# Performance work log

Measured on AMD Instinct MI355X. Metric: run time of the kernel, lower is better.

The kernel has to match this reference:

```python
import jax, jax.numpy as jnp
import numpy as np

NUM_PERSISTENT = 16
ALIBI_ALPHA = 1.0
START_I = 0
DILATION = 1
LN_EPS = 1e-5


def setup_inputs() -> dict:
    key = jax.random.key(0)
    ks = jax.random.split(key, 16)
    B, S, C, H = 8, 1024, 512, 8
    D = C // H
    P = NUM_PERSISTENT
    Kk = 3
    x = jax.random.normal(ks[0], (B, S, C), dtype=jnp.float32)
    mask = jnp.ones((B, 1, S, S), dtype=jnp.int32)
    sc = 0.02
    Wq = jax.random.normal(ks[1], (D, D), jnp.float32) * sc
    Wk = jax.random.normal(ks[2], (D, D), jnp.float32) * sc
    Wv = jax.random.normal(ks[3], (D, D), jnp.float32) * sc
    pk = jax.random.normal(ks[4], (P, H, D), jnp.float32) * sc
    pv = jax.random.normal(ks[5], (P, H, D), jnp.float32) * sc
    th_pre = jax.random.normal(ks[6], (H, H), jnp.float32) * (1.0 / np.sqrt(H))
    th_post = jax.random.normal(ks[7], (H, H), jnp.float32) * (1.0 / np.sqrt(H))
    fc_w = jax.random.normal(ks[8], (C, C), jnp.float32) * sc
    fc_b = jnp.zeros((C,), jnp.float32)
    conv1_w = jax.random.normal(ks[9], (C, C, Kk), jnp.float32) * 0.01
    conv1_b = jnp.zeros((C,), jnp.float32)
    conv2_w = jax.random.normal(ks[10], (C, C, Kk), jnp.float32) * 0.01
    conv2_b = jnp.zeros((C,), jnp.float32)
    ln_g = jnp.ones((C,), jnp.float32)
    ln_b = jnp.zeros((C,), jnp.float32)
    return dict(x=x, mask=mask, Wq=Wq, Wk=Wk, Wv=Wv, pk=pk, pv=pv,
                th_pre=th_pre, th_post=th_post, fc_w=fc_w, fc_b=fc_b,
                conv1_w=conv1_w, conv1_b=conv1_b, conv2_w=conv2_w,
                conv2_b=conv2_b, ln_g=ln_g, ln_b=ln_b)


def _causal_conv(x_nct, w_oik, b_o, dilation):
    # padding (k-1)*d on both sides + chomp right == pad left only
    k = w_oik.shape[-1]
    p = (k - 1) * dilation
    y = jax.lax.conv_general_dilated(
        x_nct, w_oik, window_strides=(1,), padding=[(p, 0)],
        rhs_dilation=(dilation,), dimension_numbers=("NCH", "OIH", "NCH"))
    return y + b_o[None, :, None]


def reference(x, mask, Wq, Wk, Wv, pk, pv, th_pre, th_post, fc_w, fc_b,
              conv1_w, conv1_b, conv2_w, conv2_b, ln_g, ln_b):
    N, S, C = x.shape
    H = th_pre.shape[0]
    D = C // H
    P = pk.shape[0]

    # ---- MultiHeadAttention (eval: dropout = identity) ----
    xh = x.reshape(N, S, H, D)
    q = jnp.einsum("nshd,ed->nshe", xh, Wq)
    k = jnp.einsum("nshd,ed->nshe", xh, Wk)
    v = jnp.einsum("nshd,ed->nshe", xh, Wv)
    # persistent memory tokens appended along key/value length
    k = jnp.concatenate([k, jnp.broadcast_to(pk[None], (N, P, H, D))], axis=1)
    v = jnp.concatenate([v, jnp.broadcast_to(pv[None], (N, P, H, D))], axis=1)

    energy = jnp.einsum("nqhd,nkhd->nhqk", q, k)  # (N,H,S,S+P)

    # ALiBi bias (symmetric |q-k|), zero over persistent keys
    slopes = 2.0 ** (-(ALIBI_ALPHA * (jnp.arange(1, H + 1, dtype=jnp.float32) + START_I)))
    t = jnp.arange(S, dtype=jnp.float32)
    dist = jnp.abs(t[:, None] - t[None, :])  # (S,S)
    bias = -dist[None, None] * slopes[None, :, None, None]  # (1,H,S,S)
    bias = jnp.pad(bias, ((0, 0), (0, 0), (0, 0), (0, P)))
    energy = energy + bias

    # pre-softmax talking heads (1x1 conv over head axis)
    energy = jnp.einsum("hg,ngqk->nhqk", th_pre, energy)

    ext_mask = jnp.pad(mask, ((0, 0), (0, 0), (0, 0), (0, P)), constant_values=1)
    energy = jnp.where(ext_mask == 0, jnp.float32(-1e4), energy)

    attn = jax.nn.softmax(energy / jnp.sqrt(jnp.float32(C)), axis=-1)
    attn = jnp.einsum("hg,ngqk->nhqk", th_post, attn)

    att_out = jnp.einsum("nhql,nlhd->nqhd", attn, v).reshape(N, S, C)
    att_out = att_out @ fc_w.T + fc_b

    x = x + att_out  # residual (dropout1 identity in eval)

    # ---- TemporalBlock (causal dilated convs, no SE since heads>0) ----
    xc = jnp.transpose(x, (0, 2, 1))  # (N,C,S)
    h = jax.nn.relu(_causal_conv(xc, conv1_w, conv1_b, DILATION))
    h = jax.nn.relu(_causal_conv(h, conv2_w, conv2_b, DILATION))
    out = jax.nn.relu(h + xc)  # downsample is None (in==out)

    # mask out invalid frames
    conv_mask = mask[:, 0, :, 0][:, None, :]  # (N,1,S)
    out = jnp.where(conv_mask == 0, 0.0, out)

    y = jnp.transpose(out, (0, 2, 1))  # (N,S,C)
    mu = jnp.mean(y, axis=-1, keepdims=True)
    var = jnp.mean(jnp.square(y - mu), axis=-1, keepdims=True)
    y = (y - mu) * jax.lax.rsqrt(var + LN_EPS) * ln_g + ln_b
    return y
```

## Files before the change

kernel.cpp:

```cpp
#include <hip/hip_runtime.h>
#include <hip/hip_bf16.h>

#define BN 8
#define SS 1024
#define CC 512
#define HH 8
#define DD 64
#define PP 16
#define KT 1040

typedef __hip_bfloat16 bf16;
typedef unsigned char uchar;
typedef unsigned short ushort;
typedef __attribute__((ext_vector_type(8))) short short8;
typedef __attribute__((ext_vector_type(4))) float f32x4;
typedef __attribute__((ext_vector_type(2))) float f32x2;

__device__ __forceinline__ short f2s(float v){ bf16 b = __float2bfloat16(v); return *(short*)&b; }
__device__ __forceinline__ float s2f(short s){ bf16 b; *(short*)&b = s; return __bfloat162float(b); }
__device__ __forceinline__ uchar f2q(float v){
    return (uchar)__builtin_amdgcn_cvt_pk_fp8_f32(v, v, 0, false);
}

#define MFMA16(a,b,c)  __builtin_amdgcn_mfma_f32_16x16x32_bf16(a,b,c,0,0,0)
#define MFMAF8(a,b,c)  __builtin_amdgcn_mfma_f32_16x16x32_fp8_fp8(a,b,c,0,0,0)

__global__ __launch_bounds__(256) void prep_kernel(
    const float* __restrict__ fc_w, const float* __restrict__ c1w,
    const float* __restrict__ c2w, const float* __restrict__ Wq,
    const float* __restrict__ Wk, const float* __restrict__ Wv,
    const float* __restrict__ th_post,
    short* __restrict__ Bfc, uchar* __restrict__ Bc1,
    uchar* __restrict__ Bc2, short* __restrict__ Bqkv)
{
    int i = blockIdx.x*256 + threadIdx.x;
    const int NFC = 512*512, NCV = 512*1536, NQ = 3*64*64;
    if (i < NFC) {
        int c = i >> 9, r = i & 511;
        int g = r >> 6, d = r & 63;
        float s = 0.f;
        #pragma unroll
        for (int h = 0; h < 8; ++h)
            s += fc_w[(size_t)c*512 + h*64 + d] * th_post[h*8 + g];
        Bfc[i] = f2s(s);
        return;
    }
    i -= NFC;
    if (i < NCV) {
        int o = i/1536, r = i%1536, dk = r>>9, ci = r&511;
        Bc1[i] = f2q(c1w[(o*512+ci)*3+dk] * 16.f); return;
    }
    i -= NCV;
    if (i < NCV) {
        int o = i/1536, r = i%1536, dk = r>>9, ci = r&511;
        Bc2[i] = f2q(c2w[(o*512+ci)*3+dk] * 16.f); return;
    }
    i -= NCV;
    if (i < NQ) {
        int w = i >> 12, rest = i & 4095;
        const float* W = (w==0)?Wq:(w==1)?Wk:Wv;
        Bqkv[i] = f2s(W[((rest>>6)&63)*64 + (rest&63)]);
    }
}

__global__ __launch_bounds__(256) void qkv_mfma(
    const float* __restrict__ x, const short* __restrict__ Bqkv,
    uchar* __restrict__ qf, uchar* __restrict__ kf, short* __restrict__ vf)
{
    __shared__ short Xs[64*72];
    __shared__ short Ws[192*72];
    const int tid = threadIdx.x;
    const int m0 = blockIdx.x * 64;
    const int h = blockIdx.y;
    const int wave = tid >> 6, lane = tid & 63;
    const int lr = lane & 15, lq = lane >> 4;

    for (int i = tid; i < 1024; i += 256) {
        int r = i >> 4, cg = (i & 15)*4;
        float4 v = *(const float4*)(x + (size_t)(m0+r)*CC + h*64 + cg);
        Xs[r*72+cg+0] = f2s(v.x); Xs[r*72+cg+1] = f2s(v.y);
        Xs[r*72+cg+2] = f2s(v.z); Xs[r*72+cg+3] = f2s(v.w);
    }
    for (int i = tid; i < 3072; i += 256) {
        int r = i >> 4, cg = (i & 15)*4;
        *(short4*)(Ws + r*72 + cg) = *(const short4*)(Bqkv + (size_t)r*64 + cg);
    }
    __syncthreads();

    f32x4 acc[12];
    #pragma unroll
    for (int nt = 0; nt < 12; ++nt) acc[nt] = {0.f,0.f,0.f,0.f};
    #pragma unroll
    for (int ks = 0; ks < 2; ++ks) {
        int ko = ks*32 + lq*8;
        short8 a = *(const short8*)(Xs + (wave*16 + lr)*72 + ko);
        #pragma unroll
        for (int nt = 0; nt < 12; ++nt) {
            short8 b = *(const short8*)(Ws + (nt*16 + lr)*72 + ko);
            acc[nt] = MFMA16(a, b, acc[nt]);
        }
    }
    #pragma unroll
    for (int nt = 0; nt < 12; ++nt) {
        int ep = nt*16 + lr;
        int w = ep >> 6, e = ep & 63;
        #pragma unroll
        for (int reg = 0; reg < 4; ++reg) {
            int m = m0 + wave*16 + lq*4 + reg;
            int n = m >> 10, s = m & 1023;
            float v = acc[nt][reg];
            if (w == 0)      qf[((size_t)(n*HH+h)*SS + s)*DD + e] = f2q(v);
            else if (w == 1) kf[((size_t)(n*HH+h)*KT + s)*DD + e] = f2q(v);
            else             vf[((size_t)(n*HH+h)*KT + s)*DD + e] = f2s(v);
        }
    }
}

__global__ __launch_bounds__(256) void persist_kernel(
    const float* __restrict__ pk, const float* __restrict__ pv,
    uchar* __restrict__ kf, short* __restrict__ vf)
{
    int idx = blockIdx.x*256 + threadIdx.x;
    if (idx >= BN*HH*PP*DD) return;
    int d = idx & 63, p = (idx >> 6) & 15, h = (idx >> 10) & 7, n = idx >> 13;
    size_t dst = (((size_t)(n*HH+h))*KT + SS + p)*DD + d;
    size_t src = ((size_t)p*HH + h)*DD + d;
    kf[dst] = f2q(pk[src]);
    vf[dst] = f2s(pv[src]);
}

__global__ __launch_bounds__(256) void vtrans_kernel(
    const short* __restrict__ vf, uchar* __restrict__ vt)
{
    __shared__ short Ts[64*65];
    const int tid = threadIdx.x;
    const int k0 = blockIdx.x * 64;
    const int nh = blockIdx.y;
    for (int i = tid; i < 1024; i += 256) {
        int kk = i >> 4, dg = (i & 15)*4;
        int k = k0 + kk;
        short4 v = {0,0,0,0};
        if (k < KT) v = *(const short4*)(vf + ((size_t)nh*KT + k)*DD + dg);
        Ts[(dg+0)*65 + kk] = v.x;
        Ts[(dg+1)*65 + kk] = v.y;
        Ts[(dg+2)*65 + kk] = v.z;
        Ts[(dg+3)*65 + kk] = v.w;
    }
    __syncthreads();
    for (int i = tid; i < 1024; i += 256) {
        int d = i >> 4, kg = (i & 15)*4;
        int k = k0 + kg;
        if (k < KT) {
            float f0 = s2f(Ts[d*65 + kg+0]), f1 = s2f(Ts[d*65 + kg+1]);
            float f2 = s2f(Ts[d*65 + kg+2]), f3 = s2f(Ts[d*65 + kg+3]);
            int p0 = __builtin_amdgcn_cvt_pk_fp8_f32(f0, f1, 0, false);
            int p1 = __builtin_amdgcn_cvt_pk_fp8_f32(f2, f3, 0, false);
            unsigned int w = (unsigned int)(p0 & 0xffff) | ((unsigned int)p1 << 16);
            *(unsigned int*)(vt + ((size_t)nh*DD + d)*KT + k) = w;
        }
    }
}

__global__ __launch_bounds__(256) void energy_mfma8(
    const uchar* __restrict__ qf, const uchar* __restrict__ kf,
    uchar* __restrict__ E)
{
    __shared__ uchar Qs[64*72];
    __shared__ uchar Ks[64*72];
    const int tid = threadIdx.x;
    const int kt = blockIdx.x;
    const int mt = blockIdx.y;
    const int nh = blockIdx.z;
    const int wave = tid >> 6, lane = tid & 63;
    const int lr = lane & 15, lq = lane >> 4;

    #pragma unroll
    for (int j = 0; j < 2; ++j) {
        int i = tid + j*256;
        int r = i >> 3, c8 = (i & 7)*8;
        *(uint2*)(Qs + r*72 + c8) =
            *(const uint2*)(qf + ((size_t)nh*SS + mt*64 + r)*DD + c8);
        int kcol = kt*64 + r;
        uint2 kv = {0u, 0u};
        if (kcol < KT)
            kv = *(const uint2*)(kf + ((size_t)nh*KT + kcol)*DD + c8);
        *(uint2*)(Ks + r*72 + c8) = kv;
    }
    __syncthreads();

    f32x4 acc[4];
    #pragma unroll
    for (int nt = 0; nt < 4; ++nt) acc[nt] = {0.f,0.f,0.f,0.f};
    #pragma unroll
    for (int ks = 0; ks < 2; ++ks) {
        int ko = ks*32 + lq*8;
        long a = *(const long*)(Qs + (wave*16 + lr)*72 + ko);
        #pragma unroll
        for (int nt = 0; nt < 4; ++nt) {
            long b = *(const long*)(Ks + (nt*16 + lr)*72 + ko);
            acc[nt] = MFMAF8(a, b, acc[nt]);
        }
    }
    const int n = nh >> 3, h = nh & 7;
    #pragma unroll
    for (int nt = 0; nt < 4; ++nt) {
        int kcol = kt*64 + nt*16 + lr;
        if (kcol >= KT) continue;
        #pragma unroll
        for (int reg = 0; reg < 4; ++reg) {
            int q = mt*64 + wave*16 + lq*4 + reg;
            E[(((size_t)(n*SS + q))*HH + h)*KT + kcol] = f2q(acc[nt][reg]);
        }
    }
}

__global__ __launch_bounds__(256) void softmax_kernel(
    uchar* __restrict__ E, const int* __restrict__ mask,
    const float* __restrict__ th_pre)
{
    __shared__ float thp[64];
    __shared__ float wred[4][8];
    const int tid = threadIdx.x;
    const int wave = tid >> 6, lane = tid & 63;
    const int blk = blockIdx.x;
    const int n = blk >> 10, q = blk & 1023;
    const float invs = 0.044194173824159216f;
    const float l2e  = 1.4426950408889634f;
    if (tid < 64) thp[tid] = th_pre[tid]*(invs*l2e);
    __syncthreads();
    uchar* Eb = E + (size_t)blk*HH*KT;

    const float sl[8] = {0.5f,0.25f,0.125f,0.0625f,
                         0.03125f,0.015625f,0.0078125f,0.00390625f};
    const int* mrow = mask + (size_t)n*SS*SS + (size_t)q*SS;

    f32x2 tp[2][8];
    float tl[8];
    float sm[8];
    #pragma unroll
    for (int g = 0; g < 8; ++g) { sm[g] = 0.f; tl[g] = 0.f; }

    #pragma unroll
    for (int jj = 0; jj < 2; ++jj) {
        const int k0 = (tid + jj*256)*2;
        const int2 mk = *(const int2*)(mrow + k0);
        const f32x2 dist = { fabsf((float)(q - k0)), fabsf((float)(q - k0 - 1)) };
        f32x2 a[8];
        #pragma unroll
        for (int g = 0; g < 8; ++g) {
            ushort u = *(const ushort*)(Eb + g*KT + k0);
            f32x2 raw = __builtin_amdgcn_cvt_pk_f32_fp8((int)u, false);
            a[g].x = raw.x - dist.x*sl[g];
            a[g].y = raw.y - dist.y*sl[g];
        }
        #pragma unroll
        for (int h = 0; h < 8; ++h) {
            f32x2 t = {0.f, 0.f};
            #pragma unroll
            for (int g = 0; g < 8; ++g) {
                float c = thp[h*8 + g];
                t.x = fmaf(c, a[g].x, t.x);
                t.y = fmaf(c, a[g].y, t.y);
            }
            f32x2 e;
            e.x = (mk.x == 0) ? 0.f : exp2f(t.x);
            e.y = (mk.y == 0) ? 0.f : exp2f(t.y);
            tp[jj][h] = e;
            sm[h] += e.x + e.y;
        }
    }
    if (tid < 16) {
        const int k = 1024 + tid;
        float a[8];
        #pragma unroll
        for (int g = 0; g < 8; ++g) {
            f32x2 r = __builtin_amdgcn_cvt_pk_f32_fp8((int)Eb[g*KT + k], false);
            a[g] = r.x;
        }
        #pragma unroll
        for (int h = 0; h < 8; ++h) {
            float t = 0.f;
            #pragma unroll
            for (int g = 0; g < 8; ++g) t = fmaf(thp[h*8 + g], a[g], t);
            float e = exp2f(t);
            tl[h] = e;
            sm[h] += e;
        }
    }
    #pragma unroll
    for (int g = 0; g < 8; ++g) {
        #pragma unroll
        for (int off = 32; off > 0; off >>= 1)
            sm[g] += __shfl_xor(sm[g], off);
    }
    if (lane == 0) {
        #pragma unroll
        for (int g = 0; g < 8; ++g) wred[wave][g] = sm[g];
    }
    __syncthreads();
    float lred[8];
    #pragma unroll
    for (int g = 0; g < 8; ++g)
        lred[g] = 1.0f / (wred[0][g] + wred[1][g] + wred[2][g] + wred[3][g]);

    #pragma unroll
    for (int jj = 0; jj < 2; ++jj) {
        const int k0 = (tid + jj*256)*2;
        #pragma unroll
        for (int g = 0; g < 8; ++g) {
            int p = __builtin_amdgcn_cvt_pk_fp8_f32(
                tp[jj][g].x * lred[g], tp[jj][g].y * lred[g], 0, false);
            *(ushort*)(Eb + g*KT + k0) = (ushort)p;
        }
    }
    if (tid < 16) {
        const int k = 1024 + tid;
        #pragma unroll
        for (int g = 0; g < 8; ++g)
            Eb[g*KT + k] = f2q(tl[g] * lred[g]);
    }
}

__device__ __forceinline__ void pv_loadP(const uchar* __restrict__ E,
    int n, int h, int ql0, int kt, int tid, uint2* rp)
{
    int r = tid >> 3, cg = (tid & 7)*8;
    int k = kt*64 + cg;
    uint2 v = {0u, 0u};
    if (k < KT)
        v = *(const uint2*)(E + (((size_t)(n*SS + ql0 + r))*HH + h)*KT + k);
    rp[0] = v;
}
__device__ __forceinline__ void pv_loadV(const uchar* __restrict__ vt,
    int nh, int kt, int tid, uint2* rv)
{
    #pragma unroll
    for (int j = 0; j < 2; ++j) {
        int i = tid + j*256;
        int r = i >> 3, cg = (i & 7)*8;
        int k = kt*64 + cg;
        uint2 v = {0u, 0u};
        if (k < KT)
            v = *(const uint2*)(vt + ((size_t)nh*DD + r)*KT + k);
        rv[j] = v;
    }
}

__global__ __launch_bounds__(256) void pv_mfma(
    const uchar* __restrict__ E, const uchar* __restrict__ vt,
    short* __restrict__ AO)
{
    __shared__ uchar Ps[32*72];
    __shared__ uchar Vs[64*72];
    const int tid = threadIdx.x;
    const int ql0 = blockIdx.x * 32;
    const int nh = blockIdx.y;
    const int n = nh >> 3, h = nh & 7;
    const int wave = tid >> 6, lane = tid & 63;
    const int lr = lane & 15, lq = lane >> 4;
    const int mh = wave & 1, nb = (wave >> 1)*32;

    uint2 rp[1], rv[2];
    pv_loadP(E, n, h, ql0, 0, tid, rp);
    pv_loadV(vt, nh, 0, tid, rv);

    f32x4 acc[2];
    acc[0] = {0.f,0.f,0.f,0.f}; acc[1] = {0.f,0.f,0.f,0.f};

    for (int kt = 0; kt < 17; ++kt) {
        if (kt) __syncthreads();
        {
            int r = tid >> 3, cg = (tid & 7)*8;
            *(uint2*)(Ps + r*72 + cg) = rp[0];
        }
        #pragma unroll
        for (int j = 0; j < 2; ++j) {
            int i = tid + j*256;
            *(uint2*)(Vs + (i >> 3)*72 + (i & 7)*8) = rv[j];
        }
        __syncthreads();
        if (kt + 1 < 17) {
            pv_loadP(E, n, h, ql0, kt+1, tid, rp);
            pv_loadV(vt, nh, kt+1, tid, rv);
        }
        #pragma unroll
        for (int ks = 0; ks < 2; ++ks) {
            int ko = ks*32 + lq*8;
            long a = *(const long*)(Ps + (mh*16 + lr)*72 + ko);
            #pragma unroll
            for (int nt = 0; nt < 2; ++nt) {
                long b = *(const long*)(Vs + (nb + nt*16 + lr)*72 + ko);
                acc[nt] = MFMAF8(a, b, acc[nt]);
            }
        }
    }
    #pragma unroll
    for (int nt = 0; nt < 2; ++nt) {
        int d = nb + nt*16 + lr;
        #pragma unroll
        for (int reg = 0; reg < 4; ++reg) {
            int qg = ql0 + mh*16 + lq*4 + reg;
            AO[((size_t)(n*SS) + qg)*CC + h*64 + d] = f2s(acc[nt][reg]);
        }
    }
}

__device__ __forceinline__ void g_load4(const short* __restrict__ src,
    size_t rowstride, int row0, int col0, int tid, short4* r)
{
    #pragma unroll
    for (int j = 0; j < 4; ++j) {
        int i = tid + j*256;
        int rr = i >> 4, cg = (i & 15)*4;
        r[j] = *(const short4*)(src + (size_t)(row0 + rr)*rowstride + col0 + cg);
    }
}
__device__ __forceinline__ void lds_store4(short* __restrict__ dst,
    int tid, const short4* r)
{
    #pragma unroll
    for (int j = 0; j < 4; ++j) {
        int i = tid + j*256;
        *(short4*)(dst + (i >> 4)*72 + (i & 15)*4) = r[j];
    }
}

__global__ __launch_bounds__(256) void fc_mfma(
    const short* __restrict__ A, const short* __restrict__ Bt,
    const float* __restrict__ bias, const float* __restrict__ x,
    short* __restrict__ out, uchar* __restrict__ out8)
{
    __shared__ short As[64*72];
    __shared__ short Bs[64*72];
    const int tid = threadIdx.x;
    const int lin = blockIdx.x + 8*blockIdx.y;
    const int xcd = lin & 7, slot = lin >> 3;
    const int m0 = (xcd*16 + (slot & 15))*64;
    const int n0 = (slot >> 4)*64;
    const int wave = tid >> 6, lane = tid & 63;
    const int lr = lane & 15, lq = lane >> 4;

    short4 ra[4], rb[4];
    g_load4(A, CC, m0, 0, tid, ra);
    g_load4(Bt, CC, n0, 0, tid, rb);

    f32x4 acc[4];
    #pragma unroll
    for (int nt = 0; nt < 4; ++nt) acc[nt] = {0.f,0.f,0.f,0.f};

    for (int kt = 0; kt < CC; kt += 64) {
        if (kt) __syncthreads();
        lds_store4(As, tid, ra);
        lds_store4(Bs, tid, rb);
        __syncthreads();
        if (kt + 64 < CC) {
            g_load4(A, CC, m0, kt+64, tid, ra);
            g_load4(Bt, CC, n0, kt+64, tid, rb);
        }
        #pragma unroll
        for (int ks = 0; ks < 2; ++ks) {
            int ko = ks*32 + lq*8;
            short8 a = *(const short8*)(As + (wave*16 + lr)*72 + ko);
            #pragma unroll
            for (int nt = 0; nt < 4; ++nt) {
                short8 b = *(const short8*)(Bs + (nt*16 + lr)*72 + ko);
                acc[nt] = MFMA16(a, b, acc[nt]);
            }
        }
    }
    #pragma unroll
    for (int nt = 0; nt < 4; ++nt) {
        int nn = n0 + nt*16 + lr;
        #pragma unroll
        for (int reg = 0; reg < 4; ++reg) {
            int m = m0 + wave*16 + lq*4 + reg;
            float v = acc[nt][reg] + bias[nn] + x[(size_t)m*CC + nn];
            out[(size_t)m*CC + nn]  = f2s(v);
            out8[(size_t)m*CC + nn] = f2q(v);
        }
    }
}

__device__ __forceinline__ void conv_loadA8(const uchar* __restrict__ A,
    int m0, int kt, int tid, uint2* ra)
{
    const int shift = (kt >> 9) - 2;
    const int ci0 = kt & 511;
    #pragma unroll
    for (int j = 0; j < 2; ++j) {
        int i = tid + j*256;
        int rr = i >> 3, c8 = (i & 7)*8;
        int m = m0 + rr;
        int s = m & (SS-1);
        uint2 v = {0u, 0u};
        if (s + shift >= 0)
            v = *(const uint2*)(A + (size_t)(m + shift)*CC + ci0 + c8);
        ra[j] = v;
    }
}
__device__ __forceinline__ void g_load8(const uchar* __restrict__ src,
    size_t rowstride, int row0, int col0, int tid, uint2* r)
{
    #pragma unroll
    for (int j = 0; j < 2; ++j) {
        int i = tid + j*256;
        int rr = i >> 3, c8 = (i & 7)*8;
        r[j] = *(const uint2*)(src + (size_t)(row0 + rr)*rowstride + col0 + c8);
    }
}
__device__ __forceinline__ void lds_store8(uchar* __restrict__ dst,
    int tid, const uint2* r)
{
    #pragma unroll
    for (int j = 0; j < 2; ++j) {
        int i = tid + j*256;
        *(uint2*)(dst + (i >> 3)*72 + (i & 7)*8) = r[j];
    }
}

__global__ __launch_bounds__(256) void conv_mfma8(
    const uchar* __restrict__ A, const uchar* __restrict__ Bt,
    const float* __restrict__ bias, uchar* __restrict__ out8,
    short* __restrict__ out16, int f8out)
{
    __shared__ uchar As[64*72];
    __shared__ uchar Bs[64*72];
    const int tid = threadIdx.x;
    const int lin = blockIdx.x + 8*blockIdx.y;
    const int xcd = lin & 7, slot = lin >> 3;
    const int m0 = (xcd*16 + (slot & 15))*64;
    const int n0 = (slot >> 4)*64;
    const int wave = tid >> 6, lane = tid & 63;
    const int lr = lane & 15, lq = lane >> 4;

    uint2 ra[2], rb[2];
    conv_loadA8(A, m0, 0, tid, ra);
    g_load8(Bt, 1536, n0, 0, tid, rb);

    f32x4 acc[4];
    #pragma unroll
    for (int nt = 0; nt < 4; ++nt) acc[nt] = {0.f,0.f,0.f,0.f};

    for (int kt = 0; kt < 1536; kt += 64) {
        if (kt) __syncthreads();
        lds_store8(As, tid, ra);
        lds_store8(Bs, tid, rb);
        __syncthreads();
        if (kt + 64 < 1536) {
            conv_loadA8(A, m0, kt+64, tid, ra);
            g_load8(Bt, 1536, n0, kt+64, tid, rb);
        }
        #pragma unroll
        for (int ks = 0; ks < 2; ++ks) {
            int ko = ks*32 + lq*8;
            long a = *(const long*)(As + (wave*16 + lr)*72 + ko);
            #pragma unroll
            for (int nt = 0; nt < 4; ++nt) {
                long b = *(const long*)(Bs + (nt*16 + lr)*72 + ko);
                acc[nt] = MFMAF8(a, b, acc[nt]);
            }
        }
    }
    #pragma unroll
    for (int nt = 0; nt < 4; ++nt) {
        int nn = n0 + nt*16 + lr;
        #pragma unroll
        for (int reg = 0; reg < 4; ++reg) {
            int m = m0 + wave*16 + lq*4 + reg;
            float v = fmaxf(acc[nt][reg]*0.0625f + bias[nn], 0.f);
            if (f8out) out8[(size_t)m*CC + nn]  = f2q(v);
            else       out16[(size_t)m*CC + nn] = f2s(v);
        }
    }
}

__global__ __launch_bounds__(256) void final_kernel(
    const short* __restrict__ c2, const short* __restrict__ xres,
    const int* __restrict__ mask, const float* __restrict__ g,
    const float* __restrict__ b, float* __restrict__ out)
{
    __shared__ float red[256];
    const int tid = threadIdx.x;
    const int m = blockIdx.x;
    const int n = m >> 10, s = m & 1023;
    const int mk = mask[(size_t)n*SS*SS + (size_t)s*SS];
    const int c0 = tid*2;

    short2 ca = *(const short2*)(c2 + (size_t)m*CC + c0);
    short2 xa = *(const short2*)(xres + (size_t)m*CC + c0);
    float v0 = fmaxf(s2f(ca.x) + s2f(xa.x), 0.f);
    float v1 = fmaxf(s2f(ca.y) + s2f(xa.y), 0.f);
    if (mk == 0) { v0 = 0.f; v1 = 0.f; }

    red[tid] = v0 + v1;
    __syncthreads();
    for (int off = 128; off > 0; off >>= 1) {
        if (tid < off) red[tid] += red[tid + off];
        __syncthreads();
    }
    float mu = red[0] * (1.0f/512.0f);
    __syncthreads();
    float d0 = v0 - mu, d1 = v1 - mu;
    red[tid] = d0*d0 + d1*d1;
    __syncthreads();
    for (int off = 128; off > 0; off >>= 1) {
        if (tid < off) red[tid] += red[tid + off];
        __syncthreads();
    }
    float rstd = rsqrtf(red[0] * (1.0f/512.0f) + 1e-5f);
    float2 gg = *(const float2*)(g + c0);
    float2 bb = *(const float2*)(b + c0);
    float2 o;
    o.x = d0*rstd*gg.x + bb.x;
    o.y = d1*rstd*gg.y + bb.y;
    *(float2*)(out + (size_t)m*CC + c0) = o;
}

extern "C" void kernel_launch(void* const* d_in, const int* in_sizes, int n_in,
                              void* d_out, int out_size, void* d_ws, size_t ws_size,
                              hipStream_t stream)
{
    const float* x      = (const float*)d_in[0];
    const int*   mask   = (const int*)  d_in[1];
    const float* Wq     = (const float*)d_in[2];
    const float* Wk     = (const float*)d_in[3];
    const float* Wv     = (const float*)d_in[4];
    const float* pk     = (const float*)d_in[5];
    const float* pv     = (const float*)d_in[6];
    const float* th_pre = (const float*)d_in[7];
    const float* th_post= (const float*)d_in[8];
    const float* fc_w   = (const float*)d_in[9];
    const float* fc_b   = (const float*)d_in[10];
    const float* c1w    = (const float*)d_in[11];
    const float* c1b    = (const float*)d_in[12];
    const float* c2w    = (const float*)d_in[13];
    const float* c2b    = (const float*)d_in[14];
    const float* lng    = (const float*)d_in[15];
    const float* lnb    = (const float*)d_in[16];
    float* out = (float*)d_out;
    (void)in_sizes; (void)n_in; (void)out_size; (void)ws_size;

    char* ws = (char*)d_ws;
    const size_t SZ_Q  = (size_t)BN*HH*SS*DD;
    const size_t SZ_K  = (size_t)BN*HH*KT*DD;
    const size_t SZ_V  = (size_t)BN*HH*KT*DD*2;
    const size_t SZ_VT = (size_t)BN*HH*DD*KT;
    const size_t SZ_E  = (size_t)BN*SS*HH*KT;
    const size_t SZ_A  = (size_t)BN*SS*CC*2;

    uchar* qf  = (uchar*)(ws);
    uchar* kf  = (uchar*)(ws + SZ_Q);
    short* vf  = (short*)(ws + SZ_Q + SZ_K);
    uchar* vt  = (uchar*)(ws + SZ_Q + SZ_K + SZ_V);
    uchar* E   = (uchar*)(ws + SZ_Q + SZ_K + SZ_V + SZ_VT);
    short* AO  = (short*)(ws + SZ_Q + SZ_K + SZ_V + SZ_VT + SZ_E);
    char*  wend = ws + SZ_Q + SZ_K + SZ_V + SZ_VT + SZ_E + SZ_A;
    short* Bfc = (short*)(wend);
    uchar* Bc1 = (uchar*)(wend + 512*512*2);
    uchar* Bc2 = (uchar*)(wend + 512*512*2 + 512*1536);
    short* Bqkv= (short*)(wend + 512*512*2 + 2*512*1536);
    uchar* xres8 = (uchar*)(wend + 512*512*2 + 2*512*1536 + 3*64*64*2);
    short* xres = (short*)(ws);
    uchar* h18  = (uchar*)E;
    short* c2   = (short*)vf;

    {
        int total = 512*512 + 2*512*1536 + 3*64*64;
        prep_kernel<<<(total + 255)/256, 256, 0, stream>>>(
            fc_w, c1w, c2w, Wq, Wk, Wv, th_post, Bfc, Bc1, Bc2, Bqkv);
    }
    qkv_mfma<<<dim3(BN*SS/64, HH), 256, 0, stream>>>(x, Bqkv, qf, kf, vf);
    persist_kernel<<<(BN*HH*PP*DD + 255)/256, 256, 0, stream>>>(pk, pv, kf, vf);
    vtrans_kernel<<<dim3(17, BN*HH), 256, 0, stream>>>(vf, vt);

    energy_mfma8<<<dim3(17, SS/64, BN*HH), 256, 0, stream>>>(qf, kf, E);
    softmax_kernel<<<BN*SS, 256, 0, stream>>>(E, mask, th_pre);
    pv_mfma<<<dim3(SS/32, BN*HH), 256, 0, stream>>>(E, vt, AO);

    fc_mfma<<<dim3(8, 128), 256, 0, stream>>>(AO, Bfc, fc_b, x, xres, xres8);
    conv_mfma8<<<dim3(8, 128), 256, 0, stream>>>(xres8, Bc1, c1b, h18, (short*)nullptr, 1);
    conv_mfma8<<<dim3(8, 128), 256, 0, stream>>>(h18, Bc2, c2b, (uchar*)nullptr, c2, 0);
    final_kernel<<<BN*SS, 256, 0, stream>>>(c2, xres, mask, lng, lnb, out);
}
```

Before: 314.8 us.

## Write transposed fp8 V directly from QKV kernel, vectorize softmax to 4 keys/thread

The QKV projection kernel now stores V directly in the transposed fp8 layout used by the PV matmul. The persistent-token kernel writes V there too, which removes the separate bf16 V buffer and the vtrans kernel launch. The softmax kernel handles four contiguous keys per thread with 32-bit loads and stores instead of two pairs of 16-bit accesses. The transposed V stores from qkv are byte-granular and strided by KT, so they are poorly coalesced, and the conv2 output buffer is moved to a new workspace region.

```diff
diff --git a/kernel.cpp b/kernel.cpp
--- a/kernel.cpp
+++ b/kernel.cpp
@@ -12,6 +12,7 @@
 typedef __hip_bfloat16 bf16;
 typedef unsigned char uchar;
 typedef unsigned short ushort;
+typedef unsigned int uint;
 typedef __attribute__((ext_vector_type(8))) short short8;
 typedef __attribute__((ext_vector_type(4))) float f32x4;
 typedef __attribute__((ext_vector_type(2))) float f32x2;
@@ -65,7 +66,7 @@
 
 __global__ __launch_bounds__(256) void qkv_mfma(
     const float* __restrict__ x, const short* __restrict__ Bqkv,
-    uchar* __restrict__ qf, uchar* __restrict__ kf, short* __restrict__ vf)
+    uchar* __restrict__ qf, uchar* __restrict__ kf, uchar* __restrict__ vt)
 {
     __shared__ short Xs[64*72];
     __shared__ short Ws[192*72];
@@ -111,54 +112,21 @@
             float v = acc[nt][reg];
             if (w == 0)      qf[((size_t)(n*HH+h)*SS + s)*DD + e] = f2q(v);
             else if (w == 1) kf[((size_t)(n*HH+h)*KT + s)*DD + e] = f2q(v);
-            else             vf[((size_t)(n*HH+h)*KT + s)*DD + e] = f2s(v);
+            else             vt[(((size_t)(n*HH+h))*DD + e)*KT + s] = f2q(v);
         }
     }
 }
 
 __global__ __launch_bounds__(256) void persist_kernel(
     const float* __restrict__ pk, const float* __restrict__ pv,
-    uchar* __restrict__ kf, short* __restrict__ vf)
+    uchar* __restrict__ kf, uchar* __restrict__ vt)
 {
     int idx = blockIdx.x*256 + threadIdx.x;
     if (idx >= BN*HH*PP*DD) return;
     int d = idx & 63, p = (idx >> 6) & 15, h = (idx >> 10) & 7, n = idx >> 13;
-    size_t dst = (((size_t)(n*HH+h))*KT + SS + p)*DD + d;
     size_t src = ((size_t)p*HH + h)*DD + d;
-    kf[dst] = f2q(pk[src]);
-    vf[dst] = f2s(pv[src]);
-}
-
-__global__ __launch_bounds__(256) void vtrans_kernel(
-    const short* __restrict__ vf, uchar* __restrict__ vt)
-{
-    __shared__ short Ts[64*65];
-    const int tid = threadIdx.x;
-    const int k0 = blockIdx.x * 64;
-    const int nh = blockIdx.y;
-    for (int i = tid; i < 1024; i += 256) {
-        int kk = i >> 4, dg = (i & 15)*4;
-        int k = k0 + kk;
-        short4 v = {0,0,0,0};
-        if (k < KT) v = *(const short4*)(vf + ((size_t)nh*KT + k)*DD + dg);
-        Ts[(dg+0)*65 + kk] = v.x;
-        Ts[(dg+1)*65 + kk] = v.y;
-        Ts[(dg+2)*65 + kk] = v.z;
-        Ts[(dg+3)*65 + kk] = v.w;
-    }
-    __syncthreads();
-    for (int i = tid; i < 1024; i += 256) {
-        int d = i >> 4, kg = (i & 15)*4;
-        int k = k0 + kg;
-        if (k < KT) {
-            float f0 = s2f(Ts[d*65 + kg+0]), f1 = s2f(Ts[d*65 + kg+1]);
-            float f2 = s2f(Ts[d*65 + kg+2]), f3 = s2f(Ts[d*65 + kg+3]);
-            int p0 = __builtin_amdgcn_cvt_pk_fp8_f32(f0, f1, 0, false);
-            int p1 = __builtin_amdgcn_cvt_pk_fp8_f32(f2, f3, 0, false);
-            unsigned int w = (unsigned int)(p0 & 0xffff) | ((unsigned int)p1 << 16);
-            *(unsigned int*)(vt + ((size_t)nh*DD + d)*KT + k) = w;
-        }
-    }
+    kf[(((size_t)(n*HH+h))*KT + SS + p)*DD + d] = f2q(pk[src]);
+    vt[(((size_t)(n*HH+h))*DD + d)*KT + SS + p] = f2q(pv[src]);
 }
 
 __global__ __launch_bounds__(256) void energy_mfma8(
@@ -234,39 +202,43 @@
                          0.03125f,0.015625f,0.0078125f,0.00390625f};
     const int* mrow = mask + (size_t)n*SS*SS + (size_t)q*SS;
 
-    f32x2 tp[2][8];
+    const int k0 = tid*4;
+    const int4 mk = *(const int4*)(mrow + k0);
+    f32x4 dist;
+    dist.x = fabsf((float)(q - k0));
+    dist.y = fabsf((float)(q - k0 - 1));
+    dist.z = fabsf((float)(q - k0 - 2));
+    dist.w = fabsf((float)(q - k0 - 3));
+
+    f32x4 tp[8];
     float tl[8];
     float sm[8];
     #pragma unroll
     for (int g = 0; g < 8; ++g) { sm[g] = 0.f; tl[g] = 0.f; }
 
-    #pragma unroll
-    for (int jj = 0; jj < 2; ++jj) {
-        const int k0 = (tid + jj*256)*2;
-        const int2 mk = *(const int2*)(mrow + k0);
-        const f32x2 dist = { fabsf((float)(q - k0)), fabsf((float)(q - k0 - 1)) };
-        f32x2 a[8];
+    {
+        f32x4 a[8];
         #pragma unroll
         for (int g = 0; g < 8; ++g) {
-            ushort u = *(const ushort*)(Eb + g*KT + k0);
-            f32x2 raw = __builtin_amdgcn_cvt_pk_f32_fp8((int)u, false);
-            a[g].x = raw.x - dist.x*sl[g];
-            a[g].y = raw.y - dist.y*sl[g];
+            uint u = *(const uint*)(Eb + g*KT + k0);
+            f32x2 lo = __builtin_amdgcn_cvt_pk_f32_fp8((int)u, false);
+            f32x2 hi = __builtin_amdgcn_cvt_pk_f32_fp8((int)u, true);
+            f32x4 r; r.x = lo.x; r.y = lo.y; r.z = hi.x; r.w = hi.y;
+            a[g] = r - dist*sl[g];
         }
         #pragma unroll
         for (int h = 0; h < 8; ++h) {
-            f32x2 t = {0.f, 0.f};
+            f32x4 t = {0.f,0.f,0.f,0.f};
             #pragma unroll
-            for (int g = 0; g < 8; ++g) {
-                float c = thp[h*8 + g];
-                t.x = fmaf(c, a[g].x, t.x);
-                t.y = fmaf(c, a[g].y, t.y);
-            }
-            f32x2 e;
+            for (int g = 0; g < 8; ++g)
+                t += a[g] * thp[h*8 + g];
+            f32x4 e;
             e.x = (mk.x == 0) ? 0.f : exp2f(t.x);
             e.y = (mk.y == 0) ? 0.f : exp2f(t.y);
-            tp[jj][h] = e;
-            sm[h] += e.x + e.y;
+            e.z = (mk.z == 0) ? 0.f : exp2f(t.z);
+            e.w = (mk.w == 0) ? 0.f : exp2f(t.w);
+            tp[h] = e;
+            sm[h] += e.x + e.y + e.z + e.w;
         }
     }
     if (tid < 16) {
@@ -304,14 +276,11 @@
         lred[g] = 1.0f / (wred[0][g] + wred[1][g] + wred[2][g] + wred[3][g]);
 
     #pragma unroll
-    for (int jj = 0; jj < 2; ++jj) {
-        const int k0 = (tid + jj*256)*2;
-        #pragma unroll
-        for (int g = 0; g < 8; ++g) {
-            int p = __builtin_amdgcn_cvt_pk_fp8_f32(
-                tp[jj][g].x * lred[g], tp[jj][g].y * lred[g], 0, false);
-            *(ushort*)(Eb + g*KT + k0) = (ushort)p;
-        }
+    for (int h = 0; h < 8; ++h) {
+        f32x4 e = tp[h] * lred[h];
+        int p = __builtin_amdgcn_cvt_pk_fp8_f32(e.x, e.y, 0, false);
+        p = __builtin_amdgcn_cvt_pk_fp8_f32(e.z, e.w, p, true);
+        *(uint*)(Eb + h*KT + k0) = (uint)p;
     }
     if (tid < 16) {
         const int k = 1024 + tid;
@@ -643,35 +612,33 @@
     char* ws = (char*)d_ws;
     const size_t SZ_Q  = (size_t)BN*HH*SS*DD;
     const size_t SZ_K  = (size_t)BN*HH*KT*DD;
-    const size_t SZ_V  = (size_t)BN*HH*KT*DD*2;
     const size_t SZ_VT = (size_t)BN*HH*DD*KT;
     const size_t SZ_E  = (size_t)BN*SS*HH*KT;
     const size_t SZ_A  = (size_t)BN*SS*CC*2;
+    const size_t SZ_A8 = (size_t)BN*SS*CC;
 
     uchar* qf  = (uchar*)(ws);
     uchar* kf  = (uchar*)(ws + SZ_Q);
-    short* vf  = (short*)(ws + SZ_Q + SZ_K);
-    uchar* vt  = (uchar*)(ws + SZ_Q + SZ_K + SZ_V);
-    uchar* E   = (uchar*)(ws + SZ_Q + SZ_K + SZ_V + SZ_VT);
-    short* AO  = (short*)(ws + SZ_Q + SZ_K + SZ_V + SZ_VT + SZ_E);
-    char*  wend = ws + SZ_Q + SZ_K + SZ_V + SZ_VT + SZ_E + SZ_A;
+    uchar* vt  = (uchar*)(ws + SZ_Q + SZ_K);
+    uchar* E   = (uchar*)(ws + SZ_Q + SZ_K + SZ_VT);
+    short* AO  = (short*)(ws + SZ_Q + SZ_K + SZ_VT + SZ_E);
+    char*  wend = ws + SZ_Q + SZ_K + SZ_VT + SZ_E + SZ_A;
     short* Bfc = (short*)(wend);
     uchar* Bc1 = (uchar*)(wend + 512*512*2);
     uchar* Bc2 = (uchar*)(wend + 512*512*2 + 512*1536);
     short* Bqkv= (short*)(wend + 512*512*2 + 2*512*1536);
     uchar* xres8 = (uchar*)(wend + 512*512*2 + 2*512*1536 + 3*64*64*2);
+    short* c2buf = (short*)(wend + 512*512*2 + 2*512*1536 + 3*64*64*2 + SZ_A8);
     short* xres = (short*)(ws);
     uchar* h18  = (uchar*)E;
-    short* c2   = (short*)vf;
 
     {
         int total = 512*512 + 2*512*1536 + 3*64*64;
         prep_kernel<<<(total + 255)/256, 256, 0, stream>>>(
             fc_w, c1w, c2w, Wq, Wk, Wv, th_post, Bfc, Bc1, Bc2, Bqkv);
     }
-    qkv_mfma<<<dim3(BN*SS/64, HH), 256, 0, stream>>>(x, Bqkv, qf, kf, vf);
-    persist_kernel<<<(BN*HH*PP*DD + 255)/256, 256, 0, stream>>>(pk, pv, kf, vf);
-    vtrans_kernel<<<dim3(17, BN*HH), 256, 0, stream>>>(vf, vt);
+    qkv_mfma<<<dim3(BN*SS/64, HH), 256, 0, stream>>>(x, Bqkv, qf, kf, vt);
+    persist_kernel<<<(BN*HH*PP*DD + 255)/256, 256, 0, stream>>>(pk, pv, kf, vt);
 
     energy_mfma8<<<dim3(17, SS/64, BN*HH), 256, 0, stream>>>(qf, kf, E);
     softmax_kernel<<<BN*SS, 256, 0, stream>>>(E, mask, th_pre);
@@ -679,6 +646,6 @@
 
     fc_mfma<<<dim3(8, 128), 256, 0, stream>>>(AO, Bfc, fc_b, x, xres, xres8);
     conv_mfma8<<<dim3(8, 128), 256, 0, stream>>>(xres8, Bc1, c1b, h18, (short*)nullptr, 1);
-    conv_mfma8<<<dim3(8, 128), 256, 0, stream>>>(h18, Bc2, c2b, (uchar*)nullptr, c2, 0);
-    final_kernel<<<BN*SS, 256, 0, stream>>>(c2, xres, mask, lng, lnb, out);
-}
+    conv_mfma8<<<dim3(8, 128), 256, 0, stream>>>(h18, Bc2, c2b, (uchar*)nullptr, c2buf, 0);
+    final_kernel<<<BN*SS, 256, 0, stream>>>(c2buf, xres, mask, lng, lnb, out);
+}
```

After: 309.1 us. Within noise of the previous version (-1.8%).
